# Performance work log

Measured on AMD Instinct MI355X. Metric: run time of the kernel, lower is better.

## Reference

```python
import jax, jax.numpy as jnp
from jax import lax
import numpy as np

NH = 8   # num_heads
WS = 7   # windowsize
SR = 2   # sr_ratio


def _conv(x, w, b, stride=1, padding=0, groups=1):
    y = lax.conv_general_dilated(x, w, (stride, stride), [(padding, padding)] * 2,
                                 dimension_numbers=('NCHW', 'OIHW', 'NCHW'),
                                 feature_group_count=groups)
    return y + b[None, :, None, None]


def _ln(x, g, b, eps=1e-5):
    m = x.mean(-1, keepdims=True)
    v = ((x - m) ** 2).mean(-1, keepdims=True)
    return (x - m) * lax.rsqrt(v + eps) * g + b


def _local_branch(q_, kv_img, dilation, stride, fc_w, sh_w, lc_w, lc_b, scale, H, W):
    # q_: [B,NH,N,hd]; kv_img: [B,C,H,W] with C = NH*hd
    B, C = kv_img.shape[0], kv_img.shape[1]
    hd = q_.shape[-1]
    pad_b = (-H) % stride
    pad_r = (-W) % stride
    kv = jnp.pad(kv_img, ((0, 0), (0, 0), (0, pad_b), (0, pad_r)), mode='reflect')
    nH, nW = (H + pad_b) // stride, (W + pad_r) // stride
    L = nH * nW
    # nn.Unfold(kernel=WS, stride, dilation): effective kernel == stride, so
    # windows tile exactly; sample each stride x stride tile at step `dilation`.
    kv = kv.reshape(B, C, nH, stride, nW, stride)[:, :, :, ::dilation, :, ::dilation]  # [B,C,nH,WS,nW,WS]
    kv = kv.transpose(0, 1, 3, 5, 2, 4).reshape(B, NH, hd, WS * WS, L)
    kv = kv.transpose(0, 1, 3, 4, 2).reshape(B, NH, WS * WS, L * hd)
    # AdaptiveAvgPool2d((None, hd)) on last dim of size L*hd -> hd buckets of L
    kv = kv.reshape(B, NH, WS * WS, hd, L).mean(-1)
    kv = (kv @ fc_w) @ sh_w                                  # [B,NH,49,2*hd]
    k_, v_ = kv[..., :hd], kv[..., hd:]
    attn = jax.nn.softmax(jnp.einsum('bhnd,bhkd->bhnk', q_, k_) * scale, axis=-1)
    v_img = v_.transpose(0, 1, 3, 2).reshape(B, C, WS, WS)
    v_ = v_ + _conv(v_img, lc_w, lc_b, padding=1, groups=C).reshape(B, NH, hd, WS * WS).transpose(0, 1, 3, 2)
    out = jnp.einsum('bhnk,bhkd->bhnd', attn, v_)            # [B,NH,N,hd]
    return out.transpose(0, 2, 1, 3).reshape(B, -1, C)


def setup_inputs() -> dict:
    key = jax.random.key(0)
    ks = jax.random.split(key, 24)
    B, H, W, dim = 2, 112, 112, 512
    N = H * W
    d0, d1, hd = 64, 224, 28
    dl = dim - d0  # 448

    def w(k, shape):
        return jax.random.normal(k, shape, jnp.float32) * 0.02

    return dict(
        x=jax.random.normal(ks[0], (B, N, dim), jnp.float32),
        Wq=w(ks[1], (dim, dim)),
        Wkv_g=w(ks[2], (d0, 2 * d0)),
        sr_w=w(ks[3], (d0, d0, SR, SR)), sr_b=w(ks[4], (d0,)),
        ln_g=jnp.ones((d0,), jnp.float32), ln_b=jnp.zeros((d0,), jnp.float32),
        lcg_w=w(ks[5], (d0, 1, 3, 3)), lcg_b=w(ks[6], (d0,)),
        kvl_dw=w(ks[7], (dl, 1, 3, 3)), kvl_db=w(ks[8], (dl,)),
        kvl_pw=w(ks[9], (dl, dl, 1, 1)), kvl_pb=w(ks[10], (dl,)),
        fc1_w=w(ks[11], (hd, hd)), sh1_w=w(ks[12], (hd, 2 * hd)),
        lc1_w=w(ks[13], (d1, 1, 3, 3)), lc1_b=w(ks[14], (d1,)),
        fc2_w=w(ks[15], (hd, hd)), sh2_w=w(ks[16], (hd, 2 * hd)),
        lc2_w=w(ks[17], (d1, 1, 3, 3)), lc2_b=w(ks[18], (d1,)),
        proj_w=w(ks[19], (dim, dim)), proj_b=w(ks[20], (dim,)),
        H=H, W=W,
    )


def reference(x, Wq, Wkv_g, sr_w, sr_b, ln_g, ln_b, lcg_w, lcg_b, kvl_dw, kvl_db,
              kvl_pw, kvl_pb, fc1_w, sh1_w, lc1_w, lc1_b, fc2_w, sh2_w, lc2_w, lc2_b,
              proj_w, proj_b, H, W):
    B, N, C = x.shape
    d0 = 64
    dl = C - d0        # 448
    hd = 224 // NH     # 28
    q = x @ Wq
    # ---- global spatially-reduced branch (1 head, dim 64) ----
    q_g = q[:, :, :d0]                                      # [B,N,64]
    x_g = x[:, :, :d0].transpose(0, 2, 1).reshape(B, d0, H, W)
    x_g = _conv(x_g, sr_w, sr_b, stride=SR)                 # [B,64,H/2,W/2]
    Hs, Ws_ = H // SR, W // SR
    Nr = Hs * Ws_
    x_g = _ln(x_g.reshape(B, d0, Nr).transpose(0, 2, 1), ln_g, ln_b)
    kvg = x_g @ Wkv_g
    k_g, v_g = kvg[..., :d0], kvg[..., d0:]
    attn_g = jax.nn.softmax(jnp.einsum('bnd,bmd->bnm', q_g, k_g) * d0 ** -0.5, axis=-1)
    v_img = v_g.transpose(0, 2, 1).reshape(B, d0, Hs, Ws_)
    v_g = v_g + _conv(v_img, lcg_w, lcg_b, padding=1, groups=d0).reshape(B, d0, Nr).transpose(0, 2, 1)
    out_g = jnp.einsum('bnm,bmd->bnd', attn_g, v_g)         # [B,N,64]
    # ---- local windowed branches (8 heads, dim 224 each) ----
    q_l = q[:, :, d0:].reshape(B, N, NH, -1).transpose(0, 2, 1, 3)  # [B,NH,N,56]
    x_l = x[:, :, d0:].reshape(B, H, W, dl).transpose(0, 3, 1, 2)
    kv_l = _conv(_conv(x_l, kvl_dw, kvl_db, padding=1, groups=dl), kvl_pw, kvl_pb)
    scale = hd ** -0.5
    out1 = _local_branch(q_l[:, :, :, :hd], kv_l[:, :224], 1, WS,
                         fc1_w, sh1_w, lc1_w, lc1_b, scale, H, W)
    out2 = _local_branch(q_l[:, :, :, hd:], kv_l[:, 224:], SR, SR * (WS - 1) + 1,
                         fc2_w, sh2_w, lc2_w, lc2_b, scale, H, W)
    return jnp.concatenate([out_g, out1, out2], -1) @ proj_w + proj_b
```

## Files before the change

### kernel.cpp

```cpp
#include <hip/hip_runtime.h>
#include <hip/hip_bf16.h>
#include <math.h>
#include <stdint.h>

static constexpr int B_    = 2;
static constexpr int N_    = 12544;
static constexpr int DIM_  = 512;
static constexpr int D0_   = 64;
static constexpr int DL_   = 448;
static constexpr int Himg  = 112;
static constexpr int Wimg  = 112;
static constexpr int HS_   = 56;
static constexpr int NR_   = 3136;
static constexpr int NH_   = 8;
static constexpr int HD_   = 28;
static constexpr int NSPLIT = 8;

typedef unsigned short ushort_t;
typedef __attribute__((ext_vector_type(8))) short short8_t;
typedef __attribute__((ext_vector_type(4))) float float4v;
typedef __attribute__((ext_vector_type(4))) unsigned uint4v;
typedef __attribute__((ext_vector_type(2))) unsigned uint2v;

static __device__ inline ushort_t bf16r(float x) {
    unsigned u = __builtin_bit_cast(unsigned, x);
    u = (u + 0x7FFFu + ((u >> 16) & 1u)) >> 16;
    return (ushort_t)u;
}
static __device__ inline float bf16tof(ushort_t h) {
    unsigned u = ((unsigned)h) << 16;
    return __builtin_bit_cast(float, u);
}
static __device__ inline unsigned pack_bf16(float lo, float hi) {
    unsigned a = __builtin_bit_cast(unsigned, lo);
    unsigned b = __builtin_bit_cast(unsigned, hi);
    a = (a + 0x7FFFu + ((a >> 16) & 1u)) >> 16;
    b = (b + 0x7FFFu + ((b >> 16) & 1u)) >> 16;
    return a | (b << 16);
}
static __device__ inline unsigned cvtpk(float lo, float hi) {
    float2 f2; f2.x = lo; f2.y = hi;
    __hip_bfloat162 h = __float22bfloat162_rn(f2);
    unsigned u;
    __builtin_memcpy(&u, &h, 4);
    return u;
}

using gptr_t = const __attribute__((address_space(1))) void*;
using lptr_t = __attribute__((address_space(3))) void*;
static __device__ inline void gload16(const void* g, void* l) {
    __builtin_amdgcn_global_load_lds((gptr_t)(uintptr_t)g, (lptr_t)(uintptr_t)l, 16, 0, 0);
}

template<bool HASBIAS, bool OUT16>
__global__ __launch_bounds__(256, 2)
void gemm_bf16_kernel(const ushort_t* __restrict__ A,
                      const ushort_t* __restrict__ Bt,
                      const float* __restrict__ bias,
                      void* __restrict__ Cv,
                      int Nn, int K, int ldc) {
    constexpr int BM = 128, BK = 64;
    __shared__ __align__(16) ushort_t As[BM * BK];
    __shared__ __align__(16) ushort_t Bs[BM * BK];
    const int bm = blockIdx.x * BM;
    const int bn = blockIdx.y * BM;
    const int tid = threadIdx.x;
    const int l15 = tid & 15;
    const int g   = (tid & 63) >> 4;
    const int w   = tid >> 6;
    const int wr  = w >> 1, wc = w & 1;

    float4v acc[4][4];
    #pragma unroll
    for (int m = 0; m < 4; ++m)
        #pragma unroll
        for (int n = 0; n < 4; ++n) acc[m][n] = (float4v){0.f, 0.f, 0.f, 0.f};

    for (int k0 = 0; k0 < K; k0 += BK) {
        #pragma unroll
        for (int i = 0; i < 4; ++i) {
            int c = i * 256 + tid;
            int r = c >> 3, ch = c & 7;
            int sch = ch ^ (r & 7);
            gload16(A  + (size_t)(bm + r) * K + k0 + sch * 8, (void*)(As + c * 8));
            gload16(Bt + (size_t)(bn + r) * K + k0 + sch * 8, (void*)(Bs + c * 8));
        }
        __syncthreads();

        short8_t af[4][2], bfr[4][2];
        #pragma unroll
        for (int m = 0; m < 4; ++m) {
            int ar = wr * 64 + m * 16 + l15;
            #pragma unroll
            for (int h = 0; h < 2; ++h)
                af[m][h] = *(const short8_t*)((const char*)As + ar * 128 + (((h * 4 + g) ^ (ar & 7)) * 16));
        }
        #pragma unroll
        for (int n = 0; n < 4; ++n) {
            int br = wc * 64 + n * 16 + l15;
            #pragma unroll
            for (int h = 0; h < 2; ++h)
                bfr[n][h] = *(const short8_t*)((const char*)Bs + br * 128 + (((h * 4 + g) ^ (br & 7)) * 16));
        }
        #pragma unroll
        for (int m = 0; m < 4; ++m)
            #pragma unroll
            for (int n = 0; n < 4; ++n) {
                acc[m][n] = __builtin_amdgcn_mfma_f32_16x16x32_bf16(af[m][0], bfr[n][0], acc[m][n], 0, 0, 0);
                acc[m][n] = __builtin_amdgcn_mfma_f32_16x16x32_bf16(af[m][1], bfr[n][1], acc[m][n], 0, 0, 0);
            }
        __syncthreads();
    }

    #pragma unroll
    for (int n = 0; n < 4; ++n) {
        int ccol = bn + wc * 64 + n * 16 + l15;
        if (ccol < Nn) {
            float bv = HASBIAS ? bias[ccol] : 0.f;
            #pragma unroll
            for (int m = 0; m < 4; ++m) {
                int crow = bm + wr * 64 + m * 16 + g * 4;
                #pragma unroll
                for (int j = 0; j < 4; ++j) {
                    float v = acc[m][n][j] + bv;
                    if (OUT16)
                        ((ushort_t*)Cv)[(size_t)(crow + j) * ldc + ccol] = bf16r(v);
                    else
                        ((float*)Cv)[(size_t)(crow + j) * ldc + ccol] = v;
                }
            }
        }
    }
}

__global__ __launch_bounds__(256)
void prep_kernel(const float* __restrict__ Wq, const float* __restrict__ kvl_pw,
                 const float* __restrict__ proj_w, const float* __restrict__ sr_w,
                 const float* __restrict__ x,
                 ushort_t* __restrict__ wqt, ushort_t* __restrict__ pwt,
                 ushort_t* __restrict__ projt, float* __restrict__ srwt,
                 ushort_t* __restrict__ xbf) {
    int idx = blockIdx.x * 256 + threadIdx.x;
    if (idx < 262144) {
        int n = idx >> 9, k = idx & 511;
        wqt[idx] = bf16r(Wq[(size_t)k * 512 + n]);
    } else if (idx < 491520) {
        int i = idx - 262144;
        int n = i / 448, k = i % 448;
        float v = (n < 448) ? kvl_pw[(size_t)n * 448 + k] : 0.f;
        pwt[i] = bf16r(v);
    } else if (idx < 753664) {
        int i = idx - 491520;
        int n = i >> 9, k = i & 511;
        projt[i] = bf16r(proj_w[(size_t)k * 512 + n]);
    } else if (idx < 770048) {
        int i = idx - 753664;
        int f = i >> 6, o2 = i & 63;
        srwt[i] = sr_w[o2 * 256 + f];
    } else {
        int i = idx - 770048;
        const float4v* p = (const float4v*)(x + (size_t)i * 8);
        float4v a = p[0], b = p[1];
        uint4v u;
        u[0] = pack_bf16(a[0], a[1]);
        u[1] = pack_bf16(a[2], a[3]);
        u[2] = pack_bf16(b[0], b[1]);
        u[3] = pack_bf16(b[2], b[3]);
        *(uint4v*)(xbf + (size_t)i * 8) = u;
    }
}

__global__ __launch_bounds__(256, 2)
void fused3_kernel(const ushort_t* __restrict__ xbf, const ushort_t* __restrict__ wqt,
                   ushort_t* __restrict__ q16,
                   const float* __restrict__ kvl_dw, const float* __restrict__ kvl_db,
                   ushort_t* __restrict__ dwtb,
                   const float* __restrict__ x, const float* __restrict__ srwt,
                   const float* __restrict__ sr_b, const float* __restrict__ ln_g,
                   const float* __restrict__ ln_b, const float* __restrict__ wkv,
                   ushort_t* __restrict__ kgb, float* __restrict__ vg) {
    const int bid = blockIdx.x;
    const int tid = threadIdx.x;
    __shared__ __align__(16) char smem[32768];

    if (bid < 784) {
        ushort_t* As = (ushort_t*)smem;
        ushort_t* Bs = (ushort_t*)(smem + 16384);
        const int bm = (bid % 196) * 128;
        const int bn = (bid / 196) * 128;
        const int l15 = tid & 15;
        const int g   = (tid & 63) >> 4;
        const int w   = tid >> 6;
        const int wr  = w >> 1, wc = w & 1;
        float4v acc[4][4];
        #pragma unroll
        for (int m = 0; m < 4; ++m)
            #pragma unroll
            for (int n = 0; n < 4; ++n) acc[m][n] = (float4v){0.f, 0.f, 0.f, 0.f};
        for (int k0 = 0; k0 < 512; k0 += 64) {
            #pragma unroll
            for (int i = 0; i < 4; ++i) {
                int c = i * 256 + tid;
                int r = c >> 3, ch = c & 7;
                int sch = ch ^ (r & 7);
                gload16(xbf + (size_t)(bm + r) * 512 + k0 + sch * 8, (void*)(As + c * 8));
                gload16(wqt + (size_t)(bn + r) * 512 + k0 + sch * 8, (void*)(Bs + c * 8));
            }
            __syncthreads();
            short8_t af[4][2], bfr[4][2];
            #pragma unroll
            for (int m = 0; m < 4; ++m) {
                int ar = wr * 64 + m * 16 + l15;
                #pragma unroll
                for (int h = 0; h < 2; ++h)
                    af[m][h] = *(const short8_t*)((const char*)As + ar * 128 + (((h * 4 + g) ^ (ar & 7)) * 16));
            }
            #pragma unroll
            for (int n = 0; n < 4; ++n) {
                int br = wc * 64 + n * 16 + l15;
                #pragma unroll
                for (int h = 0; h < 2; ++h)
                    bfr[n][h] = *(const short8_t*)((const char*)Bs + br * 128 + (((h * 4 + g) ^ (br & 7)) * 16));
            }
            #pragma unroll
            for (int m = 0; m < 4; ++m)
                #pragma unroll
                for (int n = 0; n < 4; ++n) {
                    acc[m][n] = __builtin_amdgcn_mfma_f32_16x16x32_bf16(af[m][0], bfr[n][0], acc[m][n], 0, 0, 0);
                    acc[m][n] = __builtin_amdgcn_mfma_f32_16x16x32_bf16(af[m][1], bfr[n][1], acc[m][n], 0, 0, 0);
                }
            __syncthreads();
        }
        #pragma unroll
        for (int n = 0; n < 4; ++n) {
            int ccol = bn + wc * 64 + n * 16 + l15;
            #pragma unroll
            for (int m = 0; m < 4; ++m) {
                int crow = bm + wr * 64 + m * 16 + g * 4;
                #pragma unroll
                for (int j = 0; j < 4; ++j)
                    q16[(size_t)(crow + j) * 512 + ccol] = bf16r(acc[m][n][j]);
            }
        }
    } else if (bid < 3528) {
        int idx = (bid - 784) * 256 + tid;
        int c4 = idx % 112;
        int t1 = idx / 112;
        int xx = t1 % 112;
        int t2 = t1 / 112;
        int yg = t2 % 28;
        int b  = t2 / 28;
        int c0 = c4 * 4;
        int y0 = yg * 4;
        float4v w4[9];
        #pragma unroll
        for (int kt = 0; kt < 9; ++kt) {
            w4[kt][0] = kvl_dw[(c0 + 0) * 9 + kt];
            w4[kt][1] = kvl_dw[(c0 + 1) * 9 + kt];
            w4[kt][2] = kvl_dw[(c0 + 2) * 9 + kt];
            w4[kt][3] = kvl_dw[(c0 + 3) * 9 + kt];
        }
        float4v bv = *(const float4v*)(kvl_db + c0);
        float4v acc[4];
        #pragma unroll
        for (int o2 = 0; o2 < 4; ++o2) acc[o2] = bv;
        #pragma unroll
        for (int yy = 0; yy < 6; ++yy) {
            int Y = y0 - 1 + yy;
            if (Y < 0 || Y >= Himg) continue;
            #pragma unroll
            for (int xt = 0; xt < 3; ++xt) {
                int X = xx - 1 + xt;
                if (X < 0 || X >= Wimg) continue;
                uint2v q2 = *(const uint2v*)(xbf + ((size_t)b * N_ + Y * Wimg + X) * DIM_ + D0_ + c0);
                float4v v;
                v[0] = bf16tof((ushort_t)(q2[0] & 0xffffu));
                v[1] = bf16tof((ushort_t)(q2[0] >> 16));
                v[2] = bf16tof((ushort_t)(q2[1] & 0xffffu));
                v[3] = bf16tof((ushort_t)(q2[1] >> 16));
                constexpr int olo_t[6] = {0, 0, 0, 1, 2, 3};
                constexpr int ohi_t[6] = {0, 1, 2, 3, 3, 3};
                #pragma unroll
                for (int o2 = olo_t[yy]; o2 <= ohi_t[yy]; ++o2) {
                    float4v wv = w4[(yy - o2) * 3 + xt];
                    acc[o2][0] += v[0] * wv[0];
                    acc[o2][1] += v[1] * wv[1];
                    acc[o2][2] += v[2] * wv[2];
                    acc[o2][3] += v[3] * wv[3];
                }
            }
        }
        #pragma unroll
        for (int o2 = 0; o2 < 4; ++o2) {
            uint2v pk;
            pk[0] = pack_bf16(acc[o2][0], acc[o2][1]);
            pk[1] = pack_bf16(acc[o2][2], acc[o2][3]);
            *(uint2v*)(dwtb + ((size_t)b * N_ + (y0 + o2) * Wimg + xx) * DL_ + c0) = pk;
        }
    } else {
        float* xs    = (float*)smem;
        float* lnv_s = (float*)(smem + 4096);
        const int blk4 = bid - 3528;
        const int grp  = tid >> 6;
        const int o    = tid & 63;
        const int pos  = blk4 * 4 + grp;
        const int b = pos / NR_, n = pos % NR_;
        const int y = n / HS_, xx = n % HS_;
        #pragma unroll
        for (int tap = 0; tap < 4; ++tap) {
            int ky = tap / 2, kx = tap % 2;
            xs[grp * 256 + tap * 64 + o] =
                x[((size_t)b * N_ + (2 * y + ky) * Wimg + 2 * xx + kx) * DIM_ + o];
        }
        __syncthreads();
        float sum = sr_b[o];
        for (int i = 0; i < 64; ++i) {
            const float* wr = srwt + (i * 4) * 64 + o;
            sum += xs[grp * 256 + 0 * 64 + i] * wr[0] + xs[grp * 256 + 1 * 64 + i] * wr[64]
                 + xs[grp * 256 + 2 * 64 + i] * wr[128] + xs[grp * 256 + 3 * 64 + i] * wr[192];
        }
        float m = sum;
        #pragma unroll
        for (int off = 1; off < 64; off <<= 1) m += __shfl_xor(m, off);
        m *= (1.0f / 64.0f);
        float d = sum - m;
        float v = d * d;
        #pragma unroll
        for (int off = 1; off < 64; off <<= 1) v += __shfl_xor(v, off);
        v *= (1.0f / 64.0f);
        float lnv = d * rsqrtf(v + 1e-5f) * ln_g[o] + ln_b[o];
        lnv_s[grp * 64 + o] = lnv;
        __syncthreads();
        float s0 = 0.f, s1 = 0.f;
        for (int i = 0; i < 64; ++i) {
            float lv = lnv_s[grp * 64 + i];
            s0 += lv * wkv[i * 128 + o];
            s1 += lv * wkv[i * 128 + o + 64];
        }
        const float SCK = 0.125f * 1.44269504088896340736f;
        kgb[((size_t)b * NR_ + n) * 64 + o] = bf16r(s0 * SCK);
        vg[((size_t)b * NR_ + n) * 64 + o] = s1;
    }
}

__global__ __launch_bounds__(256, 2)
void fused2_kernel(const ushort_t* __restrict__ dwtb, const ushort_t* __restrict__ pwt,
                   const float* __restrict__ kvl_pb, ushort_t* __restrict__ kvl16,
                   const float* __restrict__ vg, const float* __restrict__ lcg_w,
                   const float* __restrict__ lcg_b, ushort_t* __restrict__ vtb) {
    const int bid = blockIdx.x;
    const int tid = threadIdx.x;
    __shared__ __align__(16) char smem[32768];

    if (bid < 784) {
        ushort_t* As = (ushort_t*)smem;
        ushort_t* Bs = (ushort_t*)(smem + 16384);
        const int bm = (bid % 196) * 128;
        const int bn = (bid / 196) * 128;
        const int l15 = tid & 15;
        const int g   = (tid & 63) >> 4;
        const int w   = tid >> 6;
        const int wr  = w >> 1, wc = w & 1;
        float4v acc[4][4];
        #pragma unroll
        for (int m = 0; m < 4; ++m)
            #pragma unroll
            for (int n = 0; n < 4; ++n) acc[m][n] = (float4v){0.f, 0.f, 0.f, 0.f};
        for (int k0 = 0; k0 < 448; k0 += 64) {
            #pragma unroll
            for (int i = 0; i < 4; ++i) {
                int c = i * 256 + tid;
                int r = c >> 3, ch = c & 7;
                int sch = ch ^ (r & 7);
                gload16(dwtb + (size_t)(bm + r) * 448 + k0 + sch * 8, (void*)(As + c * 8));
                gload16(pwt  + (size_t)(bn + r) * 448 + k0 + sch * 8, (void*)(Bs + c * 8));
            }
            __syncthreads();
            short8_t af[4][2], bfr[4][2];
            #pragma unroll
            for (int m = 0; m < 4; ++m) {
                int ar = wr * 64 + m * 16 + l15;
                #pragma unroll
                for (int h = 0; h < 2; ++h)
                    af[m][h] = *(const short8_t*)((const char*)As + ar * 128 + (((h * 4 + g) ^ (ar & 7)) * 16));
            }
            #pragma unroll
            for (int n = 0; n < 4; ++n) {
                int br = wc * 64 + n * 16 + l15;
                #pragma unroll
                for (int h = 0; h < 2; ++h)
                    bfr[n][h] = *(const short8_t*)((const char*)Bs + br * 128 + (((h * 4 + g) ^ (br & 7)) * 16));
            }
            #pragma unroll
            for (int m = 0; m < 4; ++m)
                #pragma unroll
                for (int n = 0; n < 4; ++n) {
                    acc[m][n] = __builtin_amdgcn_mfma_f32_16x16x32_bf16(af[m][0], bfr[n][0], acc[m][n], 0, 0, 0);
                    acc[m][n] = __builtin_amdgcn_mfma_f32_16x16x32_bf16(af[m][1], bfr[n][1], acc[m][n], 0, 0, 0);
                }
            __syncthreads();
        }
        #pragma unroll
        for (int n = 0; n < 4; ++n) {
            int ccol = bn + wc * 64 + n * 16 + l15;
            if (ccol < 448) {
                float bv = kvl_pb[ccol];
                #pragma unroll
                for (int m = 0; m < 4; ++m) {
                    int crow = bm + wr * 64 + m * 16 + g * 4;
                    #pragma unroll
                    for (int j = 0; j < 4; ++j)
                        kvl16[(size_t)(crow + j) * 448 + ccol] = bf16r(acc[m][n][j] + bv);
                }
            }
        }
    } else {
        float* ld = (float*)smem;
        const int lb = bid - 784;
        const int b = lb / 49, n0 = (lb % 49) * 64;
        #pragma unroll
        for (int i = 0; i < 16; ++i) {
            int idx = i * 256 + tid;
            int n = idx >> 6, c = idx & 63;
            int nn = n0 + n;
            int y = nn / HS_, xx = nn % HS_;
            float sum = vg[((size_t)b * NR_ + nn) * 64 + c] + lcg_b[c];
            #pragma unroll
            for (int ky = 0; ky < 3; ++ky)
                #pragma unroll
                for (int kx = 0; kx < 3; ++kx) {
                    int yy = y + ky - 1, x2 = xx + kx - 1;
                    if (yy >= 0 && yy < HS_ && x2 >= 0 && x2 < HS_)
                        sum += vg[((size_t)b * NR_ + yy * HS_ + x2) * 64 + c] * lcg_w[c * 9 + ky * 3 + kx];
                }
            ld[n * 65 + c] = sum;
        }
        __syncthreads();
        #pragma unroll
        for (int i = 0; i < 16; ++i) {
            int idx = i * 256 + tid;
            int d = idx >> 6, nn = idx & 63;
            vtb[(size_t)(b * 64 + d) * NR_ + n0 + nn] = bf16r(ld[nn * 65 + d]);
        }
    }
}

template<int L, int NBW, int STRIDE, int DIL, int CHOFF>
__device__ inline void lm_body(int blk, int t, float* slo, float* shi,
                               const ushort_t* __restrict__ kvl16,
                               float* __restrict__ kvm) {
    const int n = blk % 49;
    const int h = (blk / 49) % NH_;
    const int b = blk / (49 * NH_);
    const int wy = n / 7, wx = n % 7;

    if (t < L) {
        const int by = t / NBW, bx = t % NBW;
        int Y = by * STRIDE + DIL * wy;
        int X = bx * STRIDE + DIL * wx;
        if (Y >= Himg) Y = 2 * Himg - 2 - Y;
        if (X >= Wimg) X = 2 * Wimg - 2 - X;
        const ushort_t* src = kvl16 + ((size_t)b * N_ + Y * Wimg + X) * DL_ + CHOFF + h * HD_;
        float v[28];
        #pragma unroll
        for (int i = 0; i < 7; ++i) {
            uint2v q2 = ((const uint2v*)src)[i];
            v[i * 4]     = bf16tof((ushort_t)(q2[0] & 0xffffu));
            v[i * 4 + 1] = bf16tof((ushort_t)(q2[0] >> 16));
            v[i * 4 + 2] = bf16tof((ushort_t)(q2[1] & 0xffffu));
            v[i * 4 + 3] = bf16tof((ushort_t)(q2[1] >> 16));
        }
        const int f0 = t * HD_;
        const int bin0 = f0 / L;
        const int nlo = min(HD_, (bin0 + 1) * L - f0);
        float s0 = 0.f, s1 = 0.f;
        #pragma unroll
        for (int j = 0; j < HD_; ++j) {
            if (j < nlo) s0 += v[j]; else s1 += v[j];
        }
        slo[t] = s0;
        shi[t] = s1;
    }
    __syncthreads();
    if (t < HD_) {
        const int t_lo = (t * L) / HD_;
        const int t_hi = min(L - 1, (t * L + L - 1) / HD_);
        float sum = 0.f;
        for (int u = t_lo; u <= t_hi; ++u) {
            int f0 = u * HD_;
            int b0 = f0 / L;
            int b1 = (f0 + HD_ - 1) / L;
            if (b0 == t) sum += slo[u];
            if (b1 == t && b1 != b0) sum += shi[u];
        }
        kvm[(size_t)blk * HD_ + t] = sum * (1.0f / (float)L);
    }
}

__global__ __launch_bounds__(512)
void fused_ag_lm_kernel(const ushort_t* __restrict__ q16,
                        const ushort_t* __restrict__ kgb,
                        const ushort_t* __restrict__ vtb,
                        ushort_t* __restrict__ osp16, float* __restrict__ mls,
                        const ushort_t* __restrict__ kvl16,
                        float* __restrict__ kvm1, float* __restrict__ kvm2) {
    const int bid = blockIdx.x;
    const int tid = threadIdx.x;
    __shared__ __align__(16) char smem[32768];
    ushort_t* Ks = (ushort_t*)smem;
    ushort_t* Vs = (ushort_t*)(smem + 16384);

    if (bid >= 1568) {
        float* slo = (float*)smem;
        float* shi = (float*)(smem + 1024);
        int lmid = bid - 1568;
        int blk = lmid % 784;
        if (lmid < 784) lm_body<256, 16, 7, 1, 0>(blk, tid, slo, shi, kvl16, kvm1);
        else            lm_body<81, 9, 13, 2, 224>(blk, tid, slo, shi, kvl16, kvm2);
        return;
    }

    const int split = (bid / 98) & 7;
    const int b     = (bid / 98) >> 3;
    const int q0    = (bid % 98) * 128;
    const int w     = tid >> 6;
    const int l     = tid & 63;
    const int l15   = l & 15;
    const int g     = l >> 4;
    const int lx    = l15 & 7;

    short8_t qf[2];
    {
        const ushort_t* qrow = q16 + ((size_t)b * N_ + q0 + w * 16 + l15) * DIM_;
        qf[0] = *(const short8_t*)(qrow + g * 8);
        qf[1] = *(const short8_t*)(qrow + g * 8 + 32);
    }

    float4v o[4];
    #pragma unroll
    for (int i = 0; i < 4; ++i) o[i] = (float4v){0.f, 0.f, 0.f, 0.f};
    float m_run = -3.0e38f, l_run = 0.f;

    const int stg_r   = tid >> 3;
    const int stg_sch = (tid & 7) ^ (stg_r & 7);
    const int stg_pr  = (stg_r & 32) | (((stg_r >> 2) & 3) << 3) | (((stg_r >> 4) & 1) << 2) | (stg_r & 3);
    auto stage = [&](int t, int buf) {
        const int k0 = t * 64;
        gload16(kgb + ((size_t)(b * NR_ + k0 + stg_pr) << 6) + stg_sch * 8,
                (void*)(Ks + buf * 4096 + tid * 8));
        gload16(vtb + (size_t)(b * 64 + stg_r) * NR_ + k0 + stg_sch * 8,
                (void*)(Vs + buf * 4096 + tid * 8));
    };

    auto compute = [&](const ushort_t* Kb, const ushort_t* Vb) {
        float4v sc[4];
        #pragma unroll
        for (int c = 0; c < 4; ++c) {
            float4v acc = (float4v){0.f, 0.f, 0.f, 0.f};
            #pragma unroll
            for (int dc = 0; dc < 2; ++dc) {
                int row = c * 16 + l15;
                short8_t ak = *(const short8_t*)((const char*)Kb + row * 128 + (((g + 4 * dc) ^ lx) * 16));
                acc = __builtin_amdgcn_mfma_f32_16x16x32_bf16(ak, qf[dc], acc, 0, 0, 0);
            }
            sc[c] = acc;
        }

        float tmax = fmaxf(fmaxf(fmaxf(sc[0][0], sc[0][1]), fmaxf(sc[0][2], sc[0][3])),
                           fmaxf(fmaxf(sc[1][0], sc[1][1]), fmaxf(sc[1][2], sc[1][3])));
        tmax = fmaxf(tmax, fmaxf(fmaxf(fmaxf(sc[2][0], sc[2][1]), fmaxf(sc[2][2], sc[2][3])),
                                 fmaxf(fmaxf(sc[3][0], sc[3][1]), fmaxf(sc[3][2], sc[3][3]))));

        if (__any(tmax > m_run + 11.0f)) {
            float rmax = fmaxf(tmax, __shfl_xor(tmax, 16));
            rmax = fmaxf(rmax, __shfl_xor(rmax, 32));
            float m_new = fmaxf(m_run, rmax);
            float corr = __builtin_amdgcn_exp2f(m_run - m_new);
            float co[4];
            #pragma unroll
            for (int r = 0; r < 4; ++r) co[r] = __shfl(corr, g * 4 + r);
            #pragma unroll
            for (int dc = 0; dc < 4; ++dc)
                #pragma unroll
                for (int r = 0; r < 4; ++r) o[dc][r] *= co[r];
            l_run *= corr;
            m_run = m_new;
        }

        float p[4][4];
        float ladd = 0.f;
        #pragma unroll
        for (int c = 0; c < 4; ++c)
            #pragma unroll
            for (int r = 0; r < 4; ++r) {
                float pe = __builtin_amdgcn_exp2f(sc[c][r] - m_run);
                p[c][r] = pe;
                ladd += pe;
            }
        l_run += ladd;

        #pragma unroll
        for (int kkc = 0; kkc < 2; ++kkc) {
            uint4v au;
            au[0] = cvtpk(p[2 * kkc][0],     p[2 * kkc][1]);
            au[1] = cvtpk(p[2 * kkc][2],     p[2 * kkc][3]);
            au[2] = cvtpk(p[2 * kkc + 1][0], p[2 * kkc + 1][1]);
            au[3] = cvtpk(p[2 * kkc + 1][2], p[2 * kkc + 1][3]);
            short8_t ap = __builtin_bit_cast(short8_t, au);
            #pragma unroll
            for (int dc = 0; dc < 4; ++dc) {
                int vrow = dc * 16 + l15;
                short8_t bv = *(const short8_t*)((const char*)Vb + vrow * 128 + (((kkc * 4 + g) ^ lx) * 16));
                o[dc] = __builtin_amdgcn_mfma_f32_16x16x32_bf16(ap, bv, o[dc], 0, 0, 0);
            }
        }
    };

    const int t0 = (split * 49) / 8;
    const int t1 = ((split + 1) * 49) / 8;
    int t = t0;
    for (; t + 1 < t1; t += 2) {
        stage(t, 0);
        stage(t + 1, 1);
        __syncthreads();
        compute(Ks, Vs);
        compute(Ks + 4096, Vs + 4096);
        __syncthreads();
    }
    if (t < t1) {
        stage(t, 0);
        __syncthreads();
        compute(Ks, Vs);
    }

    float l_tot = l_run;
    l_tot += __shfl_xor(l_tot, 16);
    l_tot += __shfl_xor(l_tot, 32);

    const size_t rbase = (size_t)(split * B_ + b) * N_;
    #pragma unroll
    for (int dc = 0; dc < 4; ++dc)
        #pragma unroll
        for (int r = 0; r < 4; ++r) {
            int row = q0 + w * 16 + g * 4 + r;
            osp16[(rbase + row) * 64 + dc * 16 + l15] = bf16r(o[dc][r]);
        }
    if (l < 16) {
        int row = q0 + w * 16 + l15;
        mls[(rbase + row) * 2]     = m_run;
        mls[(rbase + row) * 2 + 1] = l_tot;
    }
}

__global__ __launch_bounds__(256)
void fcsh_vconv_kernel(const float* __restrict__ kvm1, const float* __restrict__ fc1w,
                       const float* __restrict__ sh1w, float* __restrict__ kv1,
                       const float* __restrict__ kvm2, const float* __restrict__ fc2w,
                       const float* __restrict__ sh2w, float* __restrict__ kv2,
                       const float* __restrict__ lc1w, const float* __restrict__ lc1b,
                       float* __restrict__ v1c,
                       const float* __restrict__ lc2w, const float* __restrict__ lc2b,
                       float* __restrict__ v2c) {
    int bh2 = blockIdx.x;
    const int branch = (bh2 >= 16);
    const float* kvm = branch ? kvm2 : kvm1;
    const float* fcw = branch ? fc2w : fc1w;
    const float* shw = branch ? sh2w : sh1w;
    const float* lcw = branch ? lc2w : lc1w;
    const float* lcb = branch ? lc2b : lc1b;
    float* kvout     = branch ? kv2 : kv1;
    float* vcout     = branch ? v2c : v1c;
    int bh = branch ? bh2 - 16 : bh2;
    const int h = bh % NH_;
    __shared__ float kin[49][28];
    __shared__ float tmp[49][28];
    __shared__ float fw[28 * 28];
    __shared__ float sw[28 * 56];
    __shared__ float outs[49][56];
    int t = threadIdx.x;
    for (int i = t; i < 49 * 28; i += 256) kin[i / 28][i % 28] = kvm[bh * 49 * 28 + i];
    for (int i = t; i < 28 * 28; i += 256) fw[i] = fcw[i];
    for (int i = t; i < 28 * 56; i += 256) sw[i] = shw[i];
    __syncthreads();
    for (int i = t; i < 49 * 28; i += 256) {
        int rr = i / 28, j = i % 28;
        float s = 0.f;
        for (int k = 0; k < 28; ++k) s += kin[rr][k] * fw[k * 28 + j];
        tmp[rr][j] = s;
    }
    __syncthreads();
    for (int i = t; i < 49 * 56; i += 256) {
        int rr = i / 56, j = i % 56;
        float s = 0.f;
        for (int k = 0; k < 28; ++k) s += tmp[rr][k] * sw[k * 56 + j];
        outs[rr][j] = s;
        kvout[bh * 49 * 56 + i] = s;
    }
    __syncthreads();
    for (int i = t; i < 49 * 28; i += 256) {
        int d = i % 28, n = i / 28;
        int y = n / 7, xx = n % 7;
        int c = h * HD_ + d;
        float sum = outs[n][28 + d] + lcb[c];
        #pragma unroll
        for (int ky = 0; ky < 3; ++ky)
            #pragma unroll
            for (int kx = 0; kx < 3; ++kx) {
                int yy = y + ky - 1, x2 = xx + kx - 1;
                if (yy >= 0 && yy < 7 && x2 >= 0 && x2 < 7)
                    sum += outs[yy * 7 + x2][28 + d] * lcw[c * 9 + ky * 3 + kx];
            }
        vcout[bh * 49 * 28 + i] = sum;
    }
}

__global__ __launch_bounds__(256)
void fused_local_comb_kernel(const ushort_t* __restrict__ q16,
                             const float* __restrict__ kv1, const float* __restrict__ v1c,
                             const float* __restrict__ kv2, const float* __restrict__ v2c,
                             const ushort_t* __restrict__ osp16, const float* __restrict__ mls,
                             ushort_t* __restrict__ catb) {
    const int bid = blockIdx.x;
    const int tid = threadIdx.x;
    __shared__ __align__(16) ushort_t Ks[64 * 32];
    __shared__ __align__(16) ushort_t Vt[32 * 64];

    if (bid >= 6272) {
        int idx = (bid - 6272) * 256 + tid;
        int col = idx & 63;
        size_t rn = (size_t)(idx >> 6);
        const size_t BN = (size_t)B_ * N_;
        float ms[NSPLIT], ls[NSPLIT];
        float m = -3.0e38f;
        #pragma unroll
        for (int s = 0; s < NSPLIT; ++s) {
            ms[s] = mls[(s * BN + rn) * 2];
            ls[s] = mls[(s * BN + rn) * 2 + 1];
            m = fmaxf(m, ms[s]);
        }
        float lsum = 0.f, acc = 0.f;
        #pragma unroll
        for (int s = 0; s < NSPLIT; ++s) {
            float wgt = __builtin_amdgcn_exp2f(ms[s] - m);
            lsum += ls[s] * wgt;
            acc  += bf16tof(osp16[(s * BN + rn) * 64 + col]) * wgt;
        }
        catb[rn * DIM_ + col] = bf16r(acc / lsum);
        return;
    }

    const int ybh    = bid / 196;
    const int branch = ybh & 1;
    const int bh     = ybh >> 1;
    const int b      = bh >> 3, h = bh & 7;
    const int q0     = (bid % 196) * 64;
    const int w      = tid >> 6;
    const int l      = tid & 63;
    const int l15    = l & 15;
    const int g      = l >> 4;
    const float SC2K = 0.1889822365046136f * 1.44269504088896340736f;

    const float* kvsh = branch ? kv2 : kv1;
    const float* vc   = branch ? v2c : v1c;
    const int qoff    = D0_ + h * 56 + branch * 28;
    const int outoff  = (branch ? D0_ + 224 : D0_) + h * HD_;

    {
        int row = tid >> 2, lc = tid & 3;
        int pr = (row & 32) | (((row >> 2) & 3) << 3) | (((row >> 4) & 1) << 2) | (row & 3);
        uint4v u = (uint4v){0u, 0u, 0u, 0u};
        if (pr < 49) {
            const float* src = kvsh + (bh * 49 + pr) * 56 + lc * 8;
            float vv[8];
            #pragma unroll
            for (int j2 = 0; j2 < 8; ++j2)
                vv[j2] = (lc * 8 + j2 < 28) ? src[j2] * SC2K : 0.f;
            u[0] = cvtpk(vv[0], vv[1]);
            u[1] = cvtpk(vv[2], vv[3]);
            u[2] = cvtpk(vv[4], vv[5]);
            u[3] = cvtpk(vv[6], vv[7]);
        }
        *(uint4v*)(Ks + row * 32 + (lc ^ (row & 3)) * 8) = u;
    }
    {
        int row = tid >> 3, lc = tid & 7;
        uint4v u = (uint4v){0u, 0u, 0u, 0u};
        if (row < 28) {
            float vv[8];
            #pragma unroll
            for (int j2 = 0; j2 < 8; ++j2) {
                int kc = lc * 8 + j2;
                vv[j2] = (kc < 49) ? vc[(bh * 49 + kc) * 28 + row] : 0.f;
            }
            u[0] = cvtpk(vv[0], vv[1]);
            u[1] = cvtpk(vv[2], vv[3]);
            u[2] = cvtpk(vv[4], vv[5]);
            u[3] = cvtpk(vv[6], vv[7]);
        }
        *(uint4v*)(Vt + row * 64 + (lc ^ (row & 7)) * 8) = u;
    }
    short8_t qf;
    {
        const ushort_t* qp = q16 + ((size_t)b * N_ + q0 + w * 16 + l15) * DIM_ + qoff + g * 8;
        uint2v a01 = *(const uint2v*)qp;
        uint2v a23 = (g < 3) ? *(const uint2v*)(qp + 4) : (uint2v){0u, 0u};
        uint4v uv;
        uv[0] = a01[0]; uv[1] = a01[1]; uv[2] = a23[0]; uv[3] = a23[1];
        qf = __builtin_bit_cast(short8_t, uv);
    }
    __syncthreads();

    float4v sc4[4];
    #pragma unroll
    for (int c = 0; c < 4; ++c) {
        int row = c * 16 + l15;
        short8_t ak = *(const short8_t*)(Ks + row * 32 + ((g ^ (row & 3)) * 8));
        float4v acc = (float4v){0.f, 0.f, 0.f, 0.f};
        sc4[c] = __builtin_amdgcn_mfma_f32_16x16x32_bf16(ak, qf, acc, 0, 0, 0);
    }

    float tmax = fmaxf(fmaxf(fmaxf(sc4[0][0], sc4[0][1]), fmaxf(sc4[0][2], sc4[0][3])),
                       fmaxf(fmaxf(sc4[1][0], sc4[1][1]), fmaxf(sc4[1][2], sc4[1][3])));
    tmax = fmaxf(tmax, fmaxf(fmaxf(fmaxf(sc4[2][0], sc4[2][1]), fmaxf(sc4[2][2], sc4[2][3])),
                             fmaxf(fmaxf(sc4[3][0], sc4[3][1]), fmaxf(sc4[3][2], sc4[3][3]))));
    tmax = fmaxf(tmax, __shfl_xor(tmax, 16));
    tmax = fmaxf(tmax, __shfl_xor(tmax, 32));

    float p[4][4];
    float lsum = 0.f;
    #pragma unroll
    for (int c = 0; c < 4; ++c)
        #pragma unroll
        for (int r = 0; r < 4; ++r) {
            float pe = __builtin_amdgcn_exp2f(sc4[c][r] - tmax);
            if (c >= 2 && (8 * g + 4 * (c & 1) + r) >= 17) pe = 0.f;
            p[c][r] = pe;
            lsum += pe;
        }
    lsum += __shfl_xor(lsum, 16);
    lsum += __shfl_xor(lsum, 32);
    float inv = 1.0f / lsum;

    float4v o2[2];
    o2[0] = (float4v){0.f, 0.f, 0.f, 0.f};
    o2[1] = (float4v){0.f, 0.f, 0.f, 0.f};
    #pragma unroll
    for (int kkc = 0; kkc < 2; ++kkc) {
        uint4v au;
        au[0] = cvtpk(p[2 * kkc][0],     p[2 * kkc][1]);
        au[1] = cvtpk(p[2 * kkc][2],     p[2 * kkc][3]);
        au[2] = cvtpk(p[2 * kkc + 1][0], p[2 * kkc + 1][1]);
        au[3] = cvtpk(p[2 * kkc + 1][2], p[2 * kkc + 1][3]);
        short8_t ap = __builtin_bit_cast(short8_t, au);
        #pragma unroll
        for (int dc = 0; dc < 2; ++dc) {
            int vrow = dc * 16 + l15;
            short8_t bv = *(const short8_t*)(Vt + vrow * 64 + (((kkc * 4 + g) ^ (vrow & 7)) * 8));
            o2[dc] = __builtin_amdgcn_mfma_f32_16x16x32_bf16(ap, bv, o2[dc], 0, 0, 0);
        }
    }

    float irow[4];
    #pragma unroll
    for (int r = 0; r < 4; ++r) irow[r] = __shfl(inv, g * 4 + r);
    #pragma unroll
    for (int dc = 0; dc < 2; ++dc) {
        int d = dc * 16 + l15;
        if (d < 28) {
            #pragma unroll
            for (int r = 0; r < 4; ++r) {
                int row = q0 + w * 16 + g * 4 + r;
                catb[((size_t)b * N_ + row) * DIM_ + outoff + d] = bf16r(o2[dc][r] * irow[r]);
            }
        }
    }
}

extern "C" void kernel_launch(void* const* d_in, const int* in_sizes, int n_in,
                              void* d_out, int out_size, void* d_ws, size_t ws_size,
                              hipStream_t stream) {
    const float* x      = (const float*)d_in[0];
    const float* Wq     = (const float*)d_in[1];
    const float* Wkv_g  = (const float*)d_in[2];
    const float* sr_w   = (const float*)d_in[3];
    const float* sr_b   = (const float*)d_in[4];
    const float* ln_g   = (const float*)d_in[5];
    const float* ln_b   = (const float*)d_in[6];
    const float* lcg_w  = (const float*)d_in[7];
    const float* lcg_b  = (const float*)d_in[8];
    const float* kvl_dw = (const float*)d_in[9];
    const float* kvl_db = (const float*)d_in[10];
    const float* kvl_pw = (const float*)d_in[11];
    const float* kvl_pb = (const float*)d_in[12];
    const float* fc1_w  = (const float*)d_in[13];
    const float* sh1_w  = (const float*)d_in[14];
    const float* lc1_w  = (const float*)d_in[15];
    const float* lc1_b  = (const float*)d_in[16];
    const float* fc2_w  = (const float*)d_in[17];
    const float* sh2_w  = (const float*)d_in[18];
    const float* lc2_w  = (const float*)d_in[19];
    const float* lc2_b  = (const float*)d_in[20];
    const float* proj_w = (const float*)d_in[21];
    const float* proj_b = (const float*)d_in[22];
    float* out = (float*)d_out;
    char* base = (char*)d_ws;

    size_t o = 0;
    auto alloc = [&](size_t bytes) -> void* {
        void* p = base + o;
        o = (o + bytes + 255) & ~(size_t)255;
        return p;
    };
    ushort_t* q16   = (ushort_t*)alloc((size_t)B_ * N_ * DIM_ * 2);
    ushort_t* kvl16 = (ushort_t*)alloc((size_t)B_ * N_ * DL_ * 2);
    ushort_t* osp16 = (ushort_t*)alloc((size_t)NSPLIT * B_ * N_ * 64 * 2);
    float*    mls   = (float*)   alloc((size_t)NSPLIT * B_ * N_ * 2 * 4);
    ushort_t* xcat  = (ushort_t*)alloc((size_t)B_ * N_ * DIM_ * 2);
    ushort_t* dwtb  = (ushort_t*)alloc((size_t)B_ * N_ * DL_ * 2);
    ushort_t* kgb   = (ushort_t*)alloc((size_t)B_ * NR_ * 64 * 2);
    float*    vg    = (float*)   alloc((size_t)B_ * NR_ * 64 * 4);
    ushort_t* vtb   = (ushort_t*)alloc((size_t)B_ * 64 * NR_ * 2);
    ushort_t* wqt   = (ushort_t*)alloc((size_t)512 * 512 * 2);
    ushort_t* pwt   = (ushort_t*)alloc((size_t)512 * 448 * 2);
    ushort_t* projt = (ushort_t*)alloc((size_t)512 * 512 * 2);
    float*    srwt  = (float*)   alloc((size_t)256 * 64 * 4);
    float*    kvm1  = (float*)   alloc((size_t)B_ * NH_ * 49 * HD_ * 4);
    float*    kvm2  = (float*)   alloc((size_t)B_ * NH_ * 49 * HD_ * 4);
    float*    kv1   = (float*)   alloc((size_t)B_ * NH_ * 49 * 56 * 4);
    float*    kv2   = (float*)   alloc((size_t)B_ * NH_ * 49 * 56 * 4);
    float*    v1c   = (float*)   alloc((size_t)B_ * NH_ * 49 * HD_ * 4);
    float*    v2c   = (float*)   alloc((size_t)B_ * NH_ * 49 * HD_ * 4);
    ushort_t* xbf   = xcat;
    ushort_t* catb  = xcat;

    const int M = B_ * N_;

    prep_kernel<<<9280, 256, 0, stream>>>(Wq, kvl_pw, proj_w, sr_w, x,
                                          wqt, pwt, projt, srwt, xbf);

    fused3_kernel<<<5096, 256, 0, stream>>>(xbf, wqt, q16,
                                            kvl_dw, kvl_db, dwtb,
                                            x, srwt, sr_b, ln_g, ln_b, Wkv_g,
                                            kgb, vg);

    fused2_kernel<<<882, 256, 0, stream>>>(dwtb, pwt, kvl_pb, kvl16,
                                           vg, lcg_w, lcg_b, vtb);

    fused_ag_lm_kernel<<<3136, 512, 0, stream>>>(q16, kgb, vtb, osp16, mls,
                                                 kvl16, kvm1, kvm2);

    fcsh_vconv_kernel<<<32, 256, 0, stream>>>(kvm1, fc1_w, sh1_w, kv1,
                                              kvm2, fc2_w, sh2_w, kv2,
                                              lc1_w, lc1_b, v1c,
                                              lc2_w, lc2_b, v2c);

    fused_local_comb_kernel<<<12544, 256, 0, stream>>>(q16, kv1, v1c, kv2, v2c,
                                                       osp16, mls, catb);

    gemm_bf16_kernel<true, false><<<dim3(M / 128, 4), 256, 0, stream>>>(
        catb, projt, proj_b, out, 512, 512, 512);
}
```

Baseline: 252.7 us.

## Double-buffer LDS tiles in GEMM cores to overlap loads with MFMA

Replaces the single-buffered load-sync-compute loop in the three GEMM paths with a shared helper that ping-pongs two LDS buffers, issuing the next tile's global-to-LDS loads before computing the current one and waiting with explicit vmcnt counters. This targets exposed global memory latency in each K step. LDS per block doubles to 64 KB, which with launch bounds of 2 blocks per CU may reduce occupancy, and the hand-written waitcnt/barrier sequence adds correctness risk.

```diff
diff --git a/kernel.cpp b/kernel.cpp
--- a/kernel.cpp
+++ b/kernel.cpp
@@ -52,6 +52,74 @@
     __builtin_amdgcn_global_load_lds((gptr_t)(uintptr_t)g, (lptr_t)(uintptr_t)l, 16, 0, 0);
 }
 
+static __device__ inline void gemm_core_dbuf(const ushort_t* __restrict__ A,
+                                             const ushort_t* __restrict__ Bt,
+                                             int K, int bm, int bn, char* smem,
+                                             int tid, float4v acc[4][4]) {
+    ushort_t* As0 = (ushort_t*)smem;
+    ushort_t* Bs0 = (ushort_t*)(smem + 16384);
+    ushort_t* As1 = (ushort_t*)(smem + 32768);
+    ushort_t* Bs1 = (ushort_t*)(smem + 49152);
+    const int l15 = tid & 15;
+    const int g   = (tid & 63) >> 4;
+    const int w   = tid >> 6;
+    const int wr  = w >> 1, wc = w & 1;
+
+    auto stageT = [&](int k0, int buf) {
+        ushort_t* Ad = buf ? As1 : As0;
+        ushort_t* Bd = buf ? Bs1 : Bs0;
+        #pragma unroll
+        for (int i = 0; i < 4; ++i) {
+            int c = i * 256 + tid;
+            int r = c >> 3, ch = c & 7;
+            int sch = ch ^ (r & 7);
+            gload16(A  + (size_t)(bm + r) * K + k0 + sch * 8, (void*)(Ad + c * 8));
+            gload16(Bt + (size_t)(bn + r) * K + k0 + sch * 8, (void*)(Bd + c * 8));
+        }
+    };
+
+    const int nt = K >> 6;
+    stageT(0, 0);
+    for (int t = 0; t < nt; ++t) {
+        const int buf = t & 1;
+        if (t + 1 < nt) {
+            stageT((t + 1) << 6, buf ^ 1);
+            asm volatile("s_waitcnt vmcnt(8)" ::: "memory");
+        } else {
+            asm volatile("s_waitcnt vmcnt(0)" ::: "memory");
+        }
+        __builtin_amdgcn_sched_barrier(0);
+        __builtin_amdgcn_s_barrier();
+
+        const char* Asb = (const char*)(buf ? As1 : As0);
+        const char* Bsb = (const char*)(buf ? Bs1 : Bs0);
+        short8_t af[4][2], bfr[4][2];
+        #pragma unroll
+        for (int m = 0; m < 4; ++m) {
+            int ar = wr * 64 + m * 16 + l15;
+            #pragma unroll
+            for (int h = 0; h < 2; ++h)
+                af[m][h] = *(const short8_t*)(Asb + ar * 128 + (((h * 4 + g) ^ (ar & 7)) * 16));
+        }
+        #pragma unroll
+        for (int n = 0; n < 4; ++n) {
+            int br = wc * 64 + n * 16 + l15;
+            #pragma unroll
+            for (int h = 0; h < 2; ++h)
+                bfr[n][h] = *(const short8_t*)(Bsb + br * 128 + (((h * 4 + g) ^ (br & 7)) * 16));
+        }
+        #pragma unroll
+        for (int m = 0; m < 4; ++m)
+            #pragma unroll
+            for (int n = 0; n < 4; ++n) {
+                acc[m][n] = __builtin_amdgcn_mfma_f32_16x16x32_bf16(af[m][0], bfr[n][0], acc[m][n], 0, 0, 0);
+                acc[m][n] = __builtin_amdgcn_mfma_f32_16x16x32_bf16(af[m][1], bfr[n][1], acc[m][n], 0, 0, 0);
+            }
+        asm volatile("s_waitcnt lgkmcnt(0)" ::: "memory");
+        __builtin_amdgcn_s_barrier();
+    }
+}
+
 template<bool HASBIAS, bool OUT16>
 __global__ __launch_bounds__(256, 2)
 void gemm_bf16_kernel(const ushort_t* __restrict__ A,
@@ -59,11 +127,9 @@
                       const float* __restrict__ bias,
                       void* __restrict__ Cv,
                       int Nn, int K, int ldc) {
-    constexpr int BM = 128, BK = 64;
-    __shared__ __align__(16) ushort_t As[BM * BK];
-    __shared__ __align__(16) ushort_t Bs[BM * BK];
-    const int bm = blockIdx.x * BM;
-    const int bn = blockIdx.y * BM;
+    __shared__ __align__(16) char smem[65536];
+    const int bm = blockIdx.x * 128;
+    const int bn = blockIdx.y * 128;
     const int tid = threadIdx.x;
     const int l15 = tid & 15;
     const int g   = (tid & 63) >> 4;
@@ -76,41 +142,7 @@
         #pragma unroll
         for (int n = 0; n < 4; ++n) acc[m][n] = (float4v){0.f, 0.f, 0.f, 0.f};
 
-    for (int k0 = 0; k0 < K; k0 += BK) {
-        #pragma unroll
-        for (int i = 0; i < 4; ++i) {
-            int c = i * 256 + tid;
-            int r = c >> 3, ch = c & 7;
-            int sch = ch ^ (r & 7);
-            gload16(A  + (size_t)(bm + r) * K + k0 + sch * 8, (void*)(As + c * 8));
-            gload16(Bt + (size_t)(bn + r) * K + k0 + sch * 8, (void*)(Bs + c * 8));
-        }
-        __syncthreads();
-
-        short8_t af[4][2], bfr[4][2];
-        #pragma unroll
-        for (int m = 0; m < 4; ++m) {
-            int ar = wr * 64 + m * 16 + l15;
-            #pragma unroll
-            for (int h = 0; h < 2; ++h)
-                af[m][h] = *(const short8_t*)((const char*)As + ar * 128 + (((h * 4 + g) ^ (ar & 7)) * 16));
-        }
-        #pragma unroll
-        for (int n = 0; n < 4; ++n) {
-            int br = wc * 64 + n * 16 + l15;
-            #pragma unroll
-            for (int h = 0; h < 2; ++h)
-                bfr[n][h] = *(const short8_t*)((const char*)Bs + br * 128 + (((h * 4 + g) ^ (br & 7)) * 16));
-        }
-        #pragma unroll
-        for (int m = 0; m < 4; ++m)
-            #pragma unroll
-            for (int n = 0; n < 4; ++n) {
-                acc[m][n] = __builtin_amdgcn_mfma_f32_16x16x32_bf16(af[m][0], bfr[n][0], acc[m][n], 0, 0, 0);
-                acc[m][n] = __builtin_amdgcn_mfma_f32_16x16x32_bf16(af[m][1], bfr[n][1], acc[m][n], 0, 0, 0);
-            }
-        __syncthreads();
-    }
+    gemm_core_dbuf(A, Bt, K, bm, bn, smem, tid, acc);
 
     #pragma unroll
     for (int n = 0; n < 4; ++n) {
@@ -181,11 +213,9 @@
                    ushort_t* __restrict__ kgb, float* __restrict__ vg) {
     const int bid = blockIdx.x;
     const int tid = threadIdx.x;
-    __shared__ __align__(16) char smem[32768];
+    __shared__ __align__(16) char smem[65536];
 
     if (bid < 784) {
-        ushort_t* As = (ushort_t*)smem;
-        ushort_t* Bs = (ushort_t*)(smem + 16384);
         const int bm = (bid % 196) * 128;
         const int bn = (bid / 196) * 128;
         const int l15 = tid & 15;
@@ -197,40 +227,9 @@
         for (int m = 0; m < 4; ++m)
             #pragma unroll
             for (int n = 0; n < 4; ++n) acc[m][n] = (float4v){0.f, 0.f, 0.f, 0.f};
-        for (int k0 = 0; k0 < 512; k0 += 64) {
-            #pragma unroll
-            for (int i = 0; i < 4; ++i) {
-                int c = i * 256 + tid;
-                int r = c >> 3, ch = c & 7;
-                int sch = ch ^ (r & 7);
-                gload16(xbf + (size_t)(bm + r) * 512 + k0 + sch * 8, (void*)(As + c * 8));
-                gload16(wqt + (size_t)(bn + r) * 512 + k0 + sch * 8, (void*)(Bs + c * 8));
-            }
-            __syncthreads();
-            short8_t af[4][2], bfr[4][2];
-            #pragma unroll
-            for (int m = 0; m < 4; ++m) {
-                int ar = wr * 64 + m * 16 + l15;
-                #pragma unroll
-                for (int h = 0; h < 2; ++h)
-                    af[m][h] = *(const short8_t*)((const char*)As + ar * 128 + (((h * 4 + g) ^ (ar & 7)) * 16));
-            }
-            #pragma unroll
-            for (int n = 0; n < 4; ++n) {
-                int br = wc * 64 + n * 16 + l15;
-                #pragma unroll
-                for (int h = 0; h < 2; ++h)
-                    bfr[n][h] = *(const short8_t*)((const char*)Bs + br * 128 + (((h * 4 + g) ^ (br & 7)) * 16));
-            }
-            #pragma unroll
-            for (int m = 0; m < 4; ++m)
-                #pragma unroll
-                for (int n = 0; n < 4; ++n) {
-                    acc[m][n] = __builtin_amdgcn_mfma_f32_16x16x32_bf16(af[m][0], bfr[n][0], acc[m][n], 0, 0, 0);
-                    acc[m][n] = __builtin_amdgcn_mfma_f32_16x16x32_bf16(af[m][1], bfr[n][1], acc[m][n], 0, 0, 0);
-                }
-            __syncthreads();
-        }
+
+        gemm_core_dbuf(xbf, wqt, 512, bm, bn, smem, tid, acc);
+
         #pragma unroll
         for (int n = 0; n < 4; ++n) {
             int ccol = bn + wc * 64 + n * 16 + l15;
@@ -350,11 +349,9 @@
                    const float* __restrict__ lcg_b, ushort_t* __restrict__ vtb) {
     const int bid = blockIdx.x;
     const int tid = threadIdx.x;
-    __shared__ __align__(16) char smem[32768];
+    __shared__ __align__(16) char smem[65536];
 
     if (bid < 784) {
-        ushort_t* As = (ushort_t*)smem;
-        ushort_t* Bs = (ushort_t*)(smem + 16384);
         const int bm = (bid % 196) * 128;
         const int bn = (bid / 196) * 128;
         const int l15 = tid & 15;
@@ -366,40 +363,9 @@
         for (int m = 0; m < 4; ++m)
             #pragma unroll
             for (int n = 0; n < 4; ++n) acc[m][n] = (float4v){0.f, 0.f, 0.f, 0.f};
-        for (int k0 = 0; k0 < 448; k0 += 64) {
-            #pragma unroll
-            for (int i = 0; i < 4; ++i) {
-                int c = i * 256 + tid;
-                int r = c >> 3, ch = c & 7;
-                int sch = ch ^ (r & 7);
-                gload16(dwtb + (size_t)(bm + r) * 448 + k0 + sch * 8, (void*)(As + c * 8));
-                gload16(pwt  + (size_t)(bn + r) * 448 + k0 + sch * 8, (void*)(Bs + c * 8));
-            }
-            __syncthreads();
-            short8_t af[4][2], bfr[4][2];
-            #pragma unroll
-            for (int m = 0; m < 4; ++m) {
-                int ar = wr * 64 + m * 16 + l15;
-                #pragma unroll
-                for (int h = 0; h < 2; ++h)
-                    af[m][h] = *(const short8_t*)((const char*)As + ar * 128 + (((h * 4 + g) ^ (ar & 7)) * 16));
-            }
-            #pragma unroll
-            for (int n = 0; n < 4; ++n) {
-                int br = wc * 64 + n * 16 + l15;
-                #pragma unroll
-                for (int h = 0; h < 2; ++h)
-                    bfr[n][h] = *(const short8_t*)((const char*)Bs + br * 128 + (((h * 4 + g) ^ (br & 7)) * 16));
-            }
-            #pragma unroll
-            for (int m = 0; m < 4; ++m)
-                #pragma unroll
-                for (int n = 0; n < 4; ++n) {
-                    acc[m][n] = __builtin_amdgcn_mfma_f32_16x16x32_bf16(af[m][0], bfr[n][0], acc[m][n], 0, 0, 0);
-                    acc[m][n] = __builtin_amdgcn_mfma_f32_16x16x32_bf16(af[m][1], bfr[n][1], acc[m][n], 0, 0, 0);
-                }
-            __syncthreads();
-        }
+
+        gemm_core_dbuf(dwtb, pwt, 448, bm, bn, smem, tid, acc);
+
         #pragma unroll
         for (int n = 0; n < 4; ++n) {
             int ccol = bn + wc * 64 + n * 16 + l15;
```

Measured after the change: 264.5 us. 4.7% more time.
